# Kernel optimization log

Hardware: AMD Instinct MI355X
Metric: run time of the kernel (lower is better)

Reference implementation:

```python
import jax, jax.numpy as jnp
import numpy as np

GRID = 256      # spatial grid (periodic, pseudo-spectral)
BATCH = 8
N_STEPS = 4     # dynamics steps between outputs (layer arg N)
N_OUTPUT = 4    # number of outputs (layer arg n_output)
CH = 32         # Q_network hidden channels
DT = 0.01       # timestep
R_DRAG = 0.05   # linear (Ekman) drag
BETA = 0.5      # beta-plane coefficient
Q_SCALE = 0.01  # Q_callback scaling of network output
IN_W = 1.0      # input_weight
OUT_W = 1.0     # output_weight


def _wavenumbers():
    k = jnp.fft.fftfreq(GRID, 1.0 / GRID).astype(jnp.float32)  # integer wavenumbers
    KX = k[None, :]   # x varies along axis 1
    KY = k[:, None]   # y varies along axis 0
    K2 = KX * KX + KY * KY
    inv_lap = jnp.where(K2 > 0, -1.0 / jnp.where(K2 > 0, K2, 1.0), 0.0)  # psi_hat = -zeta_hat/k^2
    return KX, KY, inv_lap


def _q_network(z, W1, b1, W2, b2):
    # 2-layer 3x3 CNN forcing network on a single [H, W] field.
    x = z[None, :, :, None]  # NHWC
    dn = ('NHWC', 'HWIO', 'NHWC')
    h = jax.lax.conv_general_dilated(x, W1, (1, 1), 'SAME', dimension_numbers=dn) + b1
    h = jax.nn.relu(h)
    q = jax.lax.conv_general_dilated(h, W2, (1, 1), 'SAME', dimension_numbers=dn) + b2
    return q[0, :, :, 0]


def setup_inputs() -> dict:
    key = jax.random.key(0)
    k0, k1, k2, k3 = jax.random.split(key, 4)
    zeta = jax.random.normal(k0, (BATCH, GRID, GRID), dtype=jnp.float32)
    Q_0 = 0.1 * jax.random.normal(k1, (GRID, GRID), dtype=jnp.float32)
    W1 = 0.1 * jax.random.normal(k2, (3, 3, 1, CH), dtype=jnp.float32)
    b1 = jnp.zeros((CH,), dtype=jnp.float32)
    W2 = 0.1 * jax.random.normal(k3, (3, 3, CH, 1), dtype=jnp.float32)
    b2 = jnp.zeros((1,), dtype=jnp.float32)
    return {"zeta": zeta, "Q_0": Q_0, "W1": W1, "b1": b1, "W2": W2, "b2": b2}


def reference(zeta, Q_0, W1, b1, W2, b2):
    KX, KY, inv_lap = _wavenumbers()

    @jax.checkpoint
    def step(_, z):
        # Q_0 + Q_callback(dynamics, Q_network), evaluated before each step
        Q = Q_0 + Q_SCALE * _q_network(z, W1, b1, W2, b2)
        zh = jnp.fft.fft2(z)
        ph = zh * inv_lap                                  # solve nabla^2 psi = zeta
        u = jnp.real(jnp.fft.ifft2(-1j * KY * ph))         # u = -dpsi/dy
        v = jnp.real(jnp.fft.ifft2(1j * KX * ph))          # v =  dpsi/dx
        zx = jnp.real(jnp.fft.ifft2(1j * KX * zh))
        zy = jnp.real(jnp.fft.ifft2(1j * KY * zh))
        adv = u * zx + v * zy
        return z + DT * (-adv - BETA * v - R_DRAG * z + Q)

    def compute_step_outputs(z, _):
        z = jax.lax.fori_loop(0, N_STEPS, step, z)
        return z, z * OUT_W

    def compute_outputs(z0):
        _, outs = jax.lax.scan(compute_step_outputs, z0 * IN_W, None, length=N_OUTPUT)
        return outs  # [n_output, H, W]

    return jax.vmap(compute_outputs)(zeta)  # [batch, n_output, H, W]
```

## Files before the change

### kernel.cpp

```cpp
#include <hip/hip_runtime.h>

#define NG 256
#define PI2F 6.28318530717958647692f
#define PIDX(i) ((i) + ((i) >> 4))

__device__ __forceinline__ float2 f2add(float2 a, float2 b){ return make_float2(a.x+b.x, a.y+b.y); }
__device__ __forceinline__ float2 f2sub(float2 a, float2 b){ return make_float2(a.x-b.x, a.y-b.y); }
__device__ __forceinline__ float2 cmul(float2 a, float2 b){ return make_float2(a.x*b.x - a.y*b.y, a.x*b.y + a.y*b.x); }
__device__ __forceinline__ float comp(float4 v, int p) {
    return p == 0 ? v.x : p == 1 ? v.y : p == 2 ? v.z : v.w;
}
__device__ __forceinline__ float4 f4fma(float4 a, float4 v, float s) {
    return make_float4(fmaf(v.x, s, a.x), fmaf(v.y, s, a.y),
                       fmaf(v.z, s, a.z), fmaf(v.w, s, a.w));
}
__device__ __forceinline__ float dot4(float4 a, float4 b) {
    return a.x * b.x + a.y * b.y + a.z * b.z + a.w * b.w;
}

template<bool INV>
__device__ __forceinline__ void fft256_r4(float2* a, float2* b, const float2* tw,
                                          int u, bool act)
{
#pragma unroll
    for (int st = 0; st < 4; ++st) {
        if (act) {
            const int sl = 2 * st;
            const int q  = u & ((1 << sl) - 1);
            const int j1 = u - q;
            const float2 x0 = a[PIDX(u)];
            const float2 x1 = a[PIDX(u + 64)];
            const float2 x2 = a[PIDX(u + 128)];
            const float2 x3 = a[PIDX(u + 192)];
            float2 w1 = tw[j1];
            if (INV) w1.y = -w1.y;
            const float2 w2 = cmul(w1, w1);
            const float2 w3 = cmul(w1, w2);
            const float2 apc = f2add(x0, x2), amc = f2sub(x0, x2);
            const float2 bpd = f2add(x1, x3), bmd = f2sub(x1, x3);
            const float2 jb  = make_float2(-bmd.y, bmd.x);
            const float2 t0  = f2add(apc, bpd);
            const float2 t2  = f2sub(apc, bpd);
            const float2 t1  = INV ? f2add(amc, jb) : f2sub(amc, jb);
            const float2 t3  = INV ? f2sub(amc, jb) : f2add(amc, jb);
            const int wb = q + (j1 << 2);
            const int ss = 1 << sl;
            b[PIDX(wb)]          = t0;
            b[PIDX(wb + ss)]     = cmul(w1, t1);
            b[PIDX(wb + 2 * ss)] = cmul(w2, t2);
            b[PIDX(wb + 3 * ss)] = cmul(w3, t3);
        }
        __syncthreads();
        float2* tmp = a; a = b; b = tmp;
    }
}

__device__ __forceinline__ void init_tw(float2* tw, int tid)
{
    if (tid < 256) {
        float s, c;
        __sincosf(-PI2F * (float)tid * (1.f / 256.f), &s, &c);
        tw[tid] = make_float2(c, s);
    }
}

#define R_POOL 19456

__global__ void __launch_bounds__(256)
r_kernel(const float* zin, float* zout,
         const float2* __restrict__ Ct0, const float2* __restrict__ Ct1,
         float2* __restrict__ At, const float* __restrict__ Qb,
         float* __restrict__ outp, int do_d, int do_a)
{
    __shared__ __align__(16) char pool[R_POOL];
    float2* tw   = (float2*)pool;
    float2* bufs = (float2*)(pool + 2048);
    const int tid = threadIdx.x;
    const int b   = blockIdx.x >> 7;
    const int y0  = (blockIdx.x & 127) * 2;
    const int j   = tid >> 6, u = tid & 63;

    init_tw(tw, tid);

    if (do_d) {
        float2* A = bufs + j * 272;
        float2* B = bufs + (4 + j) * 272;
        const float2* src = ((j & 1) ? Ct1 : Ct0)
                          + ((size_t)(b * NG + y0 + (j >> 1))) * NG;
#pragma unroll
        for (int r4 = 0; r4 < 4; ++r4) {
            const int x = u + 64 * r4;
            A[PIDX(x)] = src[x];
        }
        __syncthreads();
        fft256_r4<true>(A, B, tw, u, true);

        const float sc = 1.f / 256.f;
        float zn01[2];
#pragma unroll
        for (int r = 0; r < 2; ++r) {
            const float2 uvv = (bufs + (2 * r) * 272)[PIDX(tid)];
            const float2 gzz = (bufs + (2 * r + 1) * 272)[PIDX(tid)];
            const float uu = uvv.x * sc, vv = uvv.y * sc;
            const float zx = gzz.x * sc, zy = gzz.y * sc;
            const int idx = (b * NG + y0 + r) * NG + tid;
            const float z0v = zin[idx];
            const float qv  = Qb[idx];
            const float adv = uu * zx + vv * zy;
            const float zn = z0v + 0.01f * (-adv - 0.5f * vv - 0.05f * z0v + qv);
            zout[idx] = zn;
            if (outp) outp[b * (4 * NG * NG) + (y0 + r) * NG + tid] = zn;
            zn01[r] = zn;
        }
        __syncthreads();
        bufs[PIDX(tid)] = make_float2(zn01[0], zn01[1]);
        __syncthreads();
    } else {
        bufs[PIDX(tid)] = make_float2(zin[(b * NG + y0) * NG + tid],
                                      zin[(b * NG + y0 + 1) * NG + tid]);
        __syncthreads();
    }

    if (do_a) {
        fft256_r4<false>(bufs, bufs + 4 * 272, tw, u, j == 0);
        const int k  = tid;
        const int km = (256 - k) & 255;
        const float2 Zk = bufs[PIDX(k)], Zm = bufs[PIDX(km)];
        const float dx = Zk.x - Zm.x, dy = Zk.y + Zm.y;
        const float4 ov = make_float4(0.5f * (Zk.x + Zm.x), 0.5f * (Zk.y - Zm.y),
                                      0.5f * dy, -0.5f * dx);
        *((float4*)(At + ((size_t)(b * NG + k)) * NG + y0)) = ov;
    }
}

#define COL_POOL 51344

__global__ void __launch_bounds__(512)
col_kernel(const float2* __restrict__ At, float2* __restrict__ Ct0,
           float2* __restrict__ Ct1, const float* __restrict__ zsrc,
           const float* __restrict__ Q0, const float* __restrict__ W1,
           const float* __restrict__ b1, const float* __restrict__ W2,
           const float* __restrict__ b2, float* __restrict__ Qb)
{
    __shared__ __align__(16) char pool[COL_POOL];
    const int tid = threadIdx.x;

    if (blockIdx.x < 2048) {
        float*  zt  = (float*)pool;
        float*  ht  = (float*)(pool + 2240);
        float4* w1s = (float4*)(pool + 48896);
        float4* w2s = (float4*)(pool + 50048);
        float*  b1s = (float*)(pool + 51200);
        float*  b2s = (float*)(pool + 51328);
        const int b   = blockIdx.x >> 8;
        const int ty0 = ((blockIdx.x >> 4) & 15) * 16, tx0 = (blockIdx.x & 15) * 16;

        if (tid < 72) {
            w1s[tid] = ((const float4*)W1)[tid];
            w2s[tid] = ((const float4*)W2)[tid];
        }
        if (tid < 32) b1s[tid] = b1[tid];
        if (tid == 0) b2s[0] = b2[0];

        for (int i = tid; i < 120; i += 512) {
            const int r = i / 6, c4 = i - r * 6;
            const int gy = ty0 - 2 + r;
            const int gx = tx0 - 4 + 4 * c4;
            float4 v = make_float4(0.f, 0.f, 0.f, 0.f);
            if ((unsigned)gy < 256u && (unsigned)gx < 256u)
                v = *((const float4*)&zsrc[(b * NG + gy) * NG + gx]);
            *((float4*)&zt[r * 28 + 4 * c4]) = v;
        }
        __syncthreads();

        if (tid < 360) {
            const int chunk = tid >> 2, cgp = tid & 3;
            const int hy = chunk / 5, hx0 = (chunk - hy * 5) * 4;
            const int k4 = hx0;
            float4 hacc[8];
#pragma unroll
            for (int c = 0; c < 8; ++c) {
                const float bv = b1s[cgp * 8 + c];
                hacc[c] = make_float4(bv, bv, bv, bv);
            }
#pragma unroll
            for (int dy = 0; dy < 3; ++dy) {
                const float* zrow = &zt[(hy + dy) * 28 + k4];
                const float4 Az = *((const float4*)zrow);
                const float4 Bz = *((const float4*)(zrow + 4));
                const float4 W0 = make_float4(Az.z, Az.w, Bz.x, Bz.y);
                const float4 W1v = make_float4(Az.w, Bz.x, Bz.y, Bz.z);
#pragma unroll
                for (int g = 0; g < 2; ++g) {
                    const float4 wa = w1s[(dy * 3 + 0) * 8 + 2 * cgp + g];
                    const float4 wb = w1s[(dy * 3 + 1) * 8 + 2 * cgp + g];
                    const float4 wc = w1s[(dy * 3 + 2) * 8 + 2 * cgp + g];
                    hacc[4*g+0] = f4fma(f4fma(f4fma(hacc[4*g+0], W0, wa.x), W1v, wb.x), Bz, wc.x);
                    hacc[4*g+1] = f4fma(f4fma(f4fma(hacc[4*g+1], W0, wa.y), W1v, wb.y), Bz, wc.y);
                    hacc[4*g+2] = f4fma(f4fma(f4fma(hacc[4*g+2], W0, wa.z), W1v, wb.z), Bz, wc.z);
                    hacc[4*g+3] = f4fma(f4fma(f4fma(hacc[4*g+3], W0, wa.w), W1v, wb.w), Bz, wc.w);
                }
            }
            const int gyh = ty0 - 1 + hy;
            const bool vy = (unsigned)gyh < 256u;
#pragma unroll
            for (int p = 0; p < 4; ++p) {
                const int hxc = hx0 + p;
                if (hxc < 18) {
                    const float mk = (vy && (unsigned)(tx0 - 1 + hxc) < 256u) ? 1.f : 0.f;
                    float* cellp = &ht[(hy * 18 + hxc) * 36];
                    const int s0 = ((2 * cgp + 0 + hxc) & 7) << 2;
                    const int s1 = ((2 * cgp + 1 + hxc) & 7) << 2;
                    const float4 lo = make_float4(
                        mk * fmaxf(comp(hacc[0], p), 0.f), mk * fmaxf(comp(hacc[1], p), 0.f),
                        mk * fmaxf(comp(hacc[2], p), 0.f), mk * fmaxf(comp(hacc[3], p), 0.f));
                    const float4 hi = make_float4(
                        mk * fmaxf(comp(hacc[4], p), 0.f), mk * fmaxf(comp(hacc[5], p), 0.f),
                        mk * fmaxf(comp(hacc[6], p), 0.f), mk * fmaxf(comp(hacc[7], p), 0.f));
                    *((float4*)(cellp + s0)) = lo;
                    *((float4*)(cellp + s1)) = hi;
                }
            }
        }
        __syncthreads();

        {
            const int chunk = tid >> 3, cg = tid & 7;
            const int oy = chunk >> 2, ox4 = (chunk & 3) * 4;
            float q0 = 0.f, q1 = 0.f, q2 = 0.f, q3 = 0.f;
#pragma unroll
            for (int dy = 0; dy < 3; ++dy) {
                const float* hrow = &ht[((oy + dy) * 18 + ox4) * 36];
                const float4 wA = w2s[(dy * 3 + 0) * 8 + cg];
                const float4 wB = w2s[(dy * 3 + 1) * 8 + cg];
                const float4 wC = w2s[(dy * 3 + 2) * 8 + cg];
#pragma unroll
                for (int jj = 0; jj < 6; ++jj) {
                    const float4 hv = *((const float4*)(hrow + jj * 36
                                        + (((cg + ox4 + jj) & 7) << 2)));
                    if (jj <= 3) {
                        const float d = dot4(hv, wA);
                        if (jj == 0) q0 += d; else if (jj == 1) q1 += d;
                        else if (jj == 2) q2 += d; else q3 += d;
                    }
                    if (jj >= 1 && jj <= 4) {
                        const float d = dot4(hv, wB);
                        if (jj == 1) q0 += d; else if (jj == 2) q1 += d;
                        else if (jj == 3) q2 += d; else q3 += d;
                    }
                    if (jj >= 2) {
                        const float d = dot4(hv, wC);
                        if (jj == 2) q0 += d; else if (jj == 3) q1 += d;
                        else if (jj == 4) q2 += d; else q3 += d;
                    }
                }
            }
#pragma unroll
            for (int s = 1; s < 8; s <<= 1) {
                q0 += __shfl_xor(q0, s); q1 += __shfl_xor(q1, s);
                q2 += __shfl_xor(q2, s); q3 += __shfl_xor(q3, s);
            }
            if (cg == 0) {
                const int gy = ty0 + oy, gx = tx0 + ox4;
                const float4 Qv = *((const float4*)&Q0[gy * NG + gx]);
                const float bb = b2s[0];
                const float4 o = make_float4(
                    Qv.x + 0.01f * (q0 + bb), Qv.y + 0.01f * (q1 + bb),
                    Qv.z + 0.01f * (q2 + bb), Qv.w + 0.01f * (q3 + bb));
                *((float4*)&Qb[(b * NG + gy) * NG + gx]) = o;
            }
        }
    } else {
        float2* tw   = (float2*)pool;
        float2* bufs = (float2*)(pool + 2048);
        const int bid = blockIdx.x - 2048;
        const int b  = bid >> 6;
        const int kg = bid & 63;
        const int j8 = tid >> 6, u = tid & 63;

        init_tw(tw, tid);
        if (j8 < 4) {
            const int kxl = 4 * kg + j8;
            float2* A = bufs + j8 * 272;
            const float2* src = At + ((size_t)(b * NG + kxl)) * NG;
#pragma unroll
            for (int r = 0; r < 4; ++r) {
                const int x = u + 64 * r;
                A[PIDX(x)] = src[x];
            }
        }
        __syncthreads();
        fft256_r4<false>(bufs + j8 * 272, bufs + (4 + (j8 & 3)) * 272, tw, u, j8 < 4);

        if (tid < 256) {
            const int jl = tid >> 6;
            const int kxl = 4 * kg + jl;
            float2* A = bufs + jl * 272;
            float2* C = bufs + (8 + jl) * 272;
            const float kxv = (kxl < 128) ? (float)kxl : (float)(kxl - 256);
            const float kxm = (kxl == 128) ? 0.f : kxv;
#pragma unroll
            for (int r = 0; r < 4; ++r) {
                const int ky = u + 64 * r;
                const float kyv = (ky < 128) ? (float)ky : (float)(ky - 256);
                const float kym = (ky == 128) ? 0.f : kyv;
                const float K2 = kxv * kxv + kyv * kyv;
                const float il = (K2 > 0.f) ? (-1.f / K2) : 0.f;
                const float2 Z = A[PIDX(ky)];
                const float ar = -kxm * il, ai = -kym * il;
                A[PIDX(ky)] = make_float2(ar * Z.x - ai * Z.y, ar * Z.y + ai * Z.x);
                C[PIDX(ky)] = make_float2(-kym * Z.x - kxm * Z.y, -kym * Z.y + kxm * Z.x);
            }
        }
        __syncthreads();

        float2* ia = (j8 < 4) ? bufs + j8 * 272 : bufs + (8 + (j8 - 4)) * 272;
        float2* ib = (j8 < 4) ? bufs + (4 + j8) * 272 : bufs + (12 + (j8 - 4)) * 272;
        fft256_r4<true>(ia, ib, tw, u, true);

        const float sc = 1.f / 256.f;
        const int y = tid & 255;
        float2 ov[4];
        if (tid < 256) {
#pragma unroll
            for (int jj = 0; jj < 4; ++jj) {
                const float2 r0 = (bufs + jj * 272)[PIDX(y)];
                ov[jj] = make_float2(r0.x * sc, r0.y * sc);
            }
            float4* dst = (float4*)(Ct0 + ((size_t)(b * NG + y)) * NG + 4 * kg);
            dst[0] = ((float4*)ov)[0];
            dst[1] = ((float4*)ov)[1];
        } else {
#pragma unroll
            for (int jj = 0; jj < 4; ++jj) {
                const float2 r1 = (bufs + (8 + jj) * 272)[PIDX(y)];
                ov[jj] = make_float2(r1.x * sc, r1.y * sc);
            }
            float4* dst = (float4*)(Ct1 + ((size_t)(b * NG + y)) * NG + 4 * kg);
            dst[0] = ((float4*)ov)[0];
            dst[1] = ((float4*)ov)[1];
        }
    }
}

extern "C" void kernel_launch(void* const* d_in, const int* in_sizes, int n_in,
                              void* d_out, int out_size, void* d_ws, size_t ws_size,
                              hipStream_t stream)
{
    const float* zeta = (const float*)d_in[0];
    const float* Q0   = (const float*)d_in[1];
    const float* W1   = (const float*)d_in[2];
    const float* b1   = (const float*)d_in[3];
    const float* W2   = (const float*)d_in[4];
    const float* b2   = (const float*)d_in[5];
    float* outp = (float*)d_out;

    char* ws = (char*)d_ws;
    float*  zws = (float*)(ws);
    float*  Qb  = (float*)(ws + (2u << 20));
    float2* At  = (float2*)(ws + (4u << 20));
    float2* Ct0 = (float2*)(ws + (8u << 20));
    float2* Ct1 = (float2*)(ws + (12u << 20));
    if (ws_size < (16u << 20)) return;

    r_kernel<<<1024, 256, 0, stream>>>(zeta, zws, Ct0, Ct1, At, Qb,
                                       nullptr, 0, 1);
    for (int j = 1; j <= 16; ++j) {
        const float* zp = (j == 1) ? zeta : zws;
        col_kernel<<<2560, 512, 0, stream>>>(At, Ct0, Ct1, zp,
                                             Q0, W1, b1, W2, b2, Qb);
        float* op = (j % 4 == 0) ? (outp + (size_t)(j / 4 - 1) * NG * NG)
                                 : nullptr;
        r_kernel<<<1024, 256, 0, stream>>>(zp, zws, Ct0, Ct1, At, Qb,
                                           op, 1, (j < 16) ? 1 : 0);
    }
}
```

Measured before the change: 602.9 us.

## Exploit Hermitian symmetry to column-FFT only half the spectrum

The row-pass forward FFT now stores only kx in 0..128 (half spectrum), and the column kernel processes 33 column groups per batch instead of 64. Each derivative field (u, v, zx, zy) goes through its own inverse column FFT into a half-width buffer G, and the row inverse FFT rebuilds the full complex row from pairs of fields using conjugate symmetry. This roughly halves the column FFT work and the intermediate traffic. The cost is more column inverse FFTs per block (two rounds), the extra kx=128 group that is mostly idle, and more complex indexing.

Result: slower. 624.1 us (+3.5%).

```diff
diff --git a/kernel.cpp b/kernel.cpp
--- a/kernel.cpp
+++ b/kernel.cpp
@@ -3,6 +3,8 @@
 #define NG 256
 #define PI2F 6.28318530717958647692f
 #define PIDX(i) ((i) + ((i) >> 4))
+#define GROW 132
+#define GF   270336
 
 __device__ __forceinline__ float2 f2add(float2 a, float2 b){ return make_float2(a.x+b.x, a.y+b.y); }
 __device__ __forceinline__ float2 f2sub(float2 a, float2 b){ return make_float2(a.x-b.x, a.y-b.y); }
@@ -68,8 +70,8 @@
 
 __global__ void __launch_bounds__(256)
 r_kernel(const float* zin, float* zout,
-         const float2* __restrict__ Ct0, const float2* __restrict__ Ct1,
-         float2* __restrict__ At, const float* __restrict__ Qb,
+         const float2* __restrict__ G, float2* __restrict__ At,
+         const float* __restrict__ Qb,
          float* __restrict__ outp, int do_d, int do_a)
 {
     __shared__ __align__(16) char pool[R_POOL];
@@ -83,14 +85,21 @@
     init_tw(tw, tid);
 
     if (do_d) {
+        const int r = j >> 1, p = j & 1;
         float2* A = bufs + j * 272;
         float2* B = bufs + (4 + j) * 272;
-        const float2* src = ((j & 1) ? Ct1 : Ct0)
-                          + ((size_t)(b * NG + y0 + (j >> 1))) * NG;
-#pragma unroll
-        for (int r4 = 0; r4 < 4; ++r4) {
-            const int x = u + 64 * r4;
-            A[PIDX(x)] = src[x];
+        const size_t rowoff = (size_t)(b * NG + y0 + r) * GROW;
+        const float2* Ga = G + (size_t)(2 * p) * GF + rowoff;
+        const float2* Gb = Ga + GF;
+        {
+            float2 ga = Ga[u], gb = Gb[u];
+            A[PIDX(u)]       = make_float2(ga.x - gb.y, ga.y + gb.x);
+            ga = Ga[u + 64]; gb = Gb[u + 64];
+            A[PIDX(u + 64)]  = make_float2(ga.x - gb.y, ga.y + gb.x);
+            ga = Ga[128 - u]; gb = Gb[128 - u];
+            A[PIDX(u + 128)] = make_float2(ga.x + gb.y, gb.x - ga.y);
+            ga = Ga[64 - u]; gb = Gb[64 - u];
+            A[PIDX(u + 192)] = make_float2(ga.x + gb.y, gb.x - ga.y);
         }
         __syncthreads();
         fft256_r4<true>(A, B, tw, u, true);
@@ -98,19 +107,19 @@
         const float sc = 1.f / 256.f;
         float zn01[2];
 #pragma unroll
-        for (int r = 0; r < 2; ++r) {
-            const float2 uvv = (bufs + (2 * r) * 272)[PIDX(tid)];
-            const float2 gzz = (bufs + (2 * r + 1) * 272)[PIDX(tid)];
+        for (int rr = 0; rr < 2; ++rr) {
+            const float2 uvv = (bufs + (2 * rr) * 272)[PIDX(tid)];
+            const float2 gzz = (bufs + (2 * rr + 1) * 272)[PIDX(tid)];
             const float uu = uvv.x * sc, vv = uvv.y * sc;
             const float zx = gzz.x * sc, zy = gzz.y * sc;
-            const int idx = (b * NG + y0 + r) * NG + tid;
+            const int idx = (b * NG + y0 + rr) * NG + tid;
             const float z0v = zin[idx];
             const float qv  = Qb[idx];
             const float adv = uu * zx + vv * zy;
             const float zn = z0v + 0.01f * (-adv - 0.5f * vv - 0.05f * z0v + qv);
             zout[idx] = zn;
-            if (outp) outp[b * (4 * NG * NG) + (y0 + r) * NG + tid] = zn;
-            zn01[r] = zn;
+            if (outp) outp[b * (4 * NG * NG) + (y0 + rr) * NG + tid] = zn;
+            zn01[rr] = zn;
         }
         __syncthreads();
         bufs[PIDX(tid)] = make_float2(zn01[0], zn01[1]);
@@ -123,21 +132,23 @@
 
     if (do_a) {
         fft256_r4<false>(bufs, bufs + 4 * 272, tw, u, j == 0);
-        const int k  = tid;
-        const int km = (256 - k) & 255;
-        const float2 Zk = bufs[PIDX(k)], Zm = bufs[PIDX(km)];
-        const float dx = Zk.x - Zm.x, dy = Zk.y + Zm.y;
-        const float4 ov = make_float4(0.5f * (Zk.x + Zm.x), 0.5f * (Zk.y - Zm.y),
-                                      0.5f * dy, -0.5f * dx);
-        *((float4*)(At + ((size_t)(b * NG + k)) * NG + y0)) = ov;
+        if (tid <= 128) {
+            const int k  = tid;
+            const int km = (256 - k) & 255;
+            const float2 Zk = bufs[PIDX(k)], Zm = bufs[PIDX(km)];
+            const float dx = Zk.x - Zm.x, dy = Zk.y + Zm.y;
+            const float4 ov = make_float4(0.5f * (Zk.x + Zm.x), 0.5f * (Zk.y - Zm.y),
+                                          0.5f * dy, -0.5f * dx);
+            *((float4*)(At + ((size_t)(b * 132 + k)) * NG + y0)) = ov;
+        }
     }
 }
 
 #define COL_POOL 51344
 
 __global__ void __launch_bounds__(512)
-col_kernel(const float2* __restrict__ At, float2* __restrict__ Ct0,
-           float2* __restrict__ Ct1, const float* __restrict__ zsrc,
+col_kernel(const float2* __restrict__ At, float2* __restrict__ G,
+           const float* __restrict__ zsrc,
            const float* __restrict__ Q0, const float* __restrict__ W1,
            const float* __restrict__ b1, const float* __restrict__ W2,
            const float* __restrict__ b2, float* __restrict__ Qb)
@@ -274,15 +285,15 @@
         float2* tw   = (float2*)pool;
         float2* bufs = (float2*)(pool + 2048);
         const int bid = blockIdx.x - 2048;
-        const int b  = bid >> 6;
-        const int kg = bid & 63;
+        const int b  = bid / 33;
+        const int kg = bid - b * 33;
         const int j8 = tid >> 6, u = tid & 63;
 
         init_tw(tw, tid);
         if (j8 < 4) {
-            const int kxl = 4 * kg + j8;
+            const int kxl = (kg == 32) ? 128 : 4 * kg + j8;
             float2* A = bufs + j8 * 272;
-            const float2* src = At + ((size_t)(b * NG + kxl)) * NG;
+            const float2* src = At + ((size_t)(b * 132 + kxl)) * NG;
 #pragma unroll
             for (int r = 0; r < 4; ++r) {
                 const int x = u + 64 * r;
@@ -292,53 +303,58 @@
         __syncthreads();
         fft256_r4<false>(bufs + j8 * 272, bufs + (4 + (j8 & 3)) * 272, tw, u, j8 < 4);
 
-        if (tid < 256) {
-            const int jl = tid >> 6;
-            const int kxl = 4 * kg + jl;
-            float2* A = bufs + jl * 272;
-            float2* C = bufs + (8 + jl) * 272;
-            const float kxv = (kxl < 128) ? (float)kxl : (float)(kxl - 256);
-            const float kxm = (kxl == 128) ? 0.f : kxv;
-#pragma unroll
-            for (int r = 0; r < 4; ++r) {
-                const int ky = u + 64 * r;
-                const float kyv = (ky < 128) ? (float)ky : (float)(ky - 256);
-                const float kym = (ky == 128) ? 0.f : kyv;
-                const float K2 = kxv * kxv + kyv * kyv;
-                const float il = (K2 > 0.f) ? (-1.f / K2) : 0.f;
-                const float2 Z = A[PIDX(ky)];
-                const float ar = -kxm * il, ai = -kym * il;
-                A[PIDX(ky)] = make_float2(ar * Z.x - ai * Z.y, ar * Z.y + ai * Z.x);
-                C[PIDX(ky)] = make_float2(-kym * Z.x - kxm * Z.y, -kym * Z.y + kxm * Z.x);
-            }
-        }
-        __syncthreads();
-
-        float2* ia = (j8 < 4) ? bufs + j8 * 272 : bufs + (8 + (j8 - 4)) * 272;
-        float2* ib = (j8 < 4) ? bufs + (4 + j8) * 272 : bufs + (12 + (j8 - 4)) * 272;
-        fft256_r4<true>(ia, ib, tw, u, true);
-
         const float sc = 1.f / 256.f;
-        const int y = tid & 255;
-        float2 ov[4];
-        if (tid < 256) {
-#pragma unroll
-            for (int jj = 0; jj < 4; ++jj) {
-                const float2 r0 = (bufs + jj * 272)[PIDX(y)];
-                ov[jj] = make_float2(r0.x * sc, r0.y * sc);
-            }
-            float4* dst = (float4*)(Ct0 + ((size_t)(b * NG + y)) * NG + 4 * kg);
-            dst[0] = ((float4*)ov)[0];
-            dst[1] = ((float4*)ov)[1];
-        } else {
-#pragma unroll
-            for (int jj = 0; jj < 4; ++jj) {
-                const float2 r1 = (bufs + (8 + jj) * 272)[PIDX(y)];
-                ov[jj] = make_float2(r1.x * sc, r1.y * sc);
-            }
-            float4* dst = (float4*)(Ct1 + ((size_t)(b * NG + y)) * NG + 4 * kg);
-            dst[0] = ((float4*)ov)[0];
-            dst[1] = ((float4*)ov)[1];
+#pragma unroll
+        for (int rd = 0; rd < 2; ++rd) {
+            {
+                const int l = j8 >> 1, fs = j8 & 1;
+                const int kxl = (kg == 32) ? 128 : 4 * kg + l;
+                const float kxv = (kxl < 128) ? (float)kxl : (float)(kxl - 256);
+                const float kxm = (kxl == 128) ? 0.f : kxv;
+                const float2* Zl = bufs + l * 272;
+                float2* S = bufs + (12 + j8) * 272;
+#pragma unroll
+                for (int r = 0; r < 4; ++r) {
+                    const int ky = u + 64 * r;
+                    const float kyv = (ky < 128) ? (float)ky : (float)(ky - 256);
+                    const float kym = (ky == 128) ? 0.f : kyv;
+                    const float K2 = kxv * kxv + kyv * kyv;
+                    const float il = (K2 > 0.f) ? (-1.f / K2) : 0.f;
+                    const float2 Z = Zl[PIDX(ky)];
+                    float2 Sv;
+                    if (rd == 0) {
+                        if (fs == 0) { const float c = kym * il; Sv = make_float2(c * Z.y, -c * Z.x); }
+                        else         { const float c = kxm * il; Sv = make_float2(-c * Z.y, c * Z.x); }
+                    } else {
+                        if (fs == 0) { Sv = make_float2(-kxm * Z.y, kxm * Z.x); }
+                        else         { Sv = make_float2(-kym * Z.y, kym * Z.x); }
+                    }
+                    S[PIDX(ky)] = Sv;
+                }
+            }
+            __syncthreads();
+            fft256_r4<true>(bufs + (12 + j8) * 272, bufs + (4 + j8) * 272, tw, u, true);
+            {
+                const int fsel = (tid >= 256) ? 1 : 0;
+                const int y = tid & 255;
+                float2* dst = G + (size_t)(2 * rd + fsel) * GF
+                            + (size_t)(b * NG + y) * GROW;
+                if (kg < 32) {
+                    float2 ov[4];
+#pragma unroll
+                    for (int l = 0; l < 4; ++l) {
+                        const float2 rv = (bufs + (12 + 2 * l + fsel) * 272)[PIDX(y)];
+                        ov[l] = make_float2(rv.x * sc, rv.y * sc);
+                    }
+                    float4* d4 = (float4*)(dst + 4 * kg);
+                    d4[0] = ((float4*)ov)[0];
+                    d4[1] = ((float4*)ov)[1];
+                } else {
+                    const float2 rv = (bufs + (12 + fsel) * 272)[PIDX(y)];
+                    dst[128] = make_float2(rv.x * sc, rv.y * sc);
+                }
+            }
+            __syncthreads();
         }
     }
 }
@@ -359,19 +375,16 @@
     float*  zws = (float*)(ws);
     float*  Qb  = (float*)(ws + (2u << 20));
     float2* At  = (float2*)(ws + (4u << 20));
-    float2* Ct0 = (float2*)(ws + (8u << 20));
-    float2* Ct1 = (float2*)(ws + (12u << 20));
-    if (ws_size < (16u << 20)) return;
-
-    r_kernel<<<1024, 256, 0, stream>>>(zeta, zws, Ct0, Ct1, At, Qb,
-                                       nullptr, 0, 1);
+    float2* G   = (float2*)(ws + 6815744u);
+    if (ws_size < 15466496u) return;
+
+    r_kernel<<<1024, 256, 0, stream>>>(zeta, zws, G, At, Qb, nullptr, 0, 1);
     for (int j = 1; j <= 16; ++j) {
         const float* zp = (j == 1) ? zeta : zws;
-        col_kernel<<<2560, 512, 0, stream>>>(At, Ct0, Ct1, zp,
-                                             Q0, W1, b1, W2, b2, Qb);
+        col_kernel<<<2312, 512, 0, stream>>>(At, G, zp, Q0, W1, b1, W2, b2, Qb);
         float* op = (j % 4 == 0) ? (outp + (size_t)(j / 4 - 1) * NG * NG)
                                  : nullptr;
-        r_kernel<<<1024, 256, 0, stream>>>(zp, zws, Ct0, Ct1, At, Qb,
+        r_kernel<<<1024, 256, 0, stream>>>(zp, zws, G, At, Qb,
                                            op, 1, (j < 16) ? 1 : 0);
     }
 }
```
